# Optimization experiments

Hardware: AMD Instinct MI355X
Metric: run time of the kernel (lower is better)

## Reference

```python
import jax, jax.numpy as jnp
import numpy as np
from jax import lax

B, C_IN, C_HID, NUM_CLASSES, HW = 128, 256, 1024, 1, 17
DN = ('NCHW', 'OIHW', 'NCHW')


def setup_inputs() -> dict:
    key = jax.random.key(0)
    k = jax.random.split(key, 5)
    x = jax.random.normal(k[0], (B, C_IN, HW, HW), dtype=jnp.float32)
    # ConvRnn stand-in: 3x3 SAME conv 256->1024 + tanh (zero initial hidden state)
    w_rnn = jax.random.normal(k[1], (C_HID, C_IN, 3, 3), dtype=jnp.float32) * 0.02
    b_rnn = jax.random.normal(k[2], (C_HID,), dtype=jnp.float32) * 0.02
    # 1x1 conv 1024 -> NUM_CLASSES
    w_out = jax.random.normal(k[3], (NUM_CLASSES, C_HID, 1, 1), dtype=jnp.float32) * 0.02
    b_out = jax.random.normal(k[4], (NUM_CLASSES,), dtype=jnp.float32) * 0.02
    return {"x": x, "w_rnn": w_rnn, "b_rnn": b_rnn, "w_out": w_out, "b_out": b_out}


def _branch(x, w_rnn, b_rnn, w_out, b_out):
    h = jnp.tanh(
        lax.conv_general_dilated(x, w_rnn, (1, 1), 'SAME', dimension_numbers=DN)
        + b_rnn[None, :, None, None]
    )
    h = jax.nn.relu(h)
    s = lax.conv_general_dilated(h, w_out, (1, 1), 'SAME', dimension_numbers=DN)
    return jax.nn.sigmoid(s + b_out[None, :, None, None])  # [B, NUM_CLASSES, 17, 17]


def reference(x, w_rnn, b_rnn, w_out, b_out):
    score = _branch(x, w_rnn, b_rnn, w_out, b_out)
    # per-sample peak of channel-0 map; first occurrence in row-major order
    flat = score[:, 0].reshape(score.shape[0], -1)          # [B, H*W]
    idx = jnp.argmax(flat, axis=-1)                          # first max, like nonzero()[0]
    pos_list = jnp.stack([idx // HW, idx % HW], axis=-1).astype(jnp.int32)  # [B, 2] = (y, x)
    return (score, pos_list)
```

## Files before the change

### kernel.cpp

```cpp
#include <hip/hip_runtime.h>
#include <hip/hip_bf16.h>

#define HW_ 17
#define P_ 289
#define BIMG 128
#define CIN 256
#define CHID 1024

#define WS_ZERO_OFF 0
#define WS_S_OFF    1024
#define WS_W2_OFF   262144
#define WS_X2_OFF   9699328

typedef __attribute__((ext_vector_type(8))) short short8;
typedef __attribute__((ext_vector_type(4))) float float4_t;

__device__ __forceinline__ unsigned short f32_to_bf16_rne(float f) {
  unsigned int u = __builtin_bit_cast(unsigned int, f);
  unsigned int r = (u + 0x7FFFu + ((u >> 16) & 1u)) >> 16;
  return (unsigned short)r;
}
__device__ __forceinline__ float bf16_bits_to_f32(unsigned short h) {
  unsigned int u = ((unsigned int)h) << 16;
  return __builtin_bit_cast(float, u);
}

__device__ __forceinline__ void glds16(const void* g, void* l) {
  __builtin_amdgcn_global_load_lds(
      (const __attribute__((address_space(1))) void*)g,
      (__attribute__((address_space(3))) void*)l, 16, 0, 0);
}

__global__ void prep_w_kernel(const float* __restrict__ w_rnn,
                              unsigned short* __restrict__ w2) {
  int t = blockIdx.x * 256 + threadIdx.x;
  int c = t & 255;
  int oc = (t >> 8) & 1023;
  int kyx = t >> 18;
  float w = w_rnn[(size_t)(oc * 256 + c) * 9 + kyx];
  unsigned short hi = f32_to_bf16_rne(w);
  unsigned short lo = f32_to_bf16_rne(w - bf16_bits_to_f32(hi));
  size_t base = (size_t)(kyx * 1024 + oc) * 512;
  w2[base + c] = hi;
  w2[base + 256 + c] = lo;
}

__global__ void prep_x_kernel(const float* __restrict__ x,
                              unsigned short* __restrict__ x2) {
  __shared__ unsigned short hibuf[P_ * 34];
  __shared__ unsigned short lobuf[P_ * 34];
  int n = blockIdx.y;
  int c0 = blockIdx.x * 32;
  int t = threadIdx.x;
  for (int ci = 0; ci < 32; ++ci) {
    const float* src = x + (size_t)(n * CIN + c0 + ci) * P_;
    for (int pb = 0; pb < 2; ++pb) {
      int p = pb * 256 + t;
      if (p < P_) {
        float v = src[p];
        unsigned short h = f32_to_bf16_rne(v);
        hibuf[p * 34 + ci] = h;
        lobuf[p * 34 + ci] = f32_to_bf16_rne(v - bf16_bits_to_f32(h));
      }
    }
  }
  __syncthreads();
  int ci = t & 31;
  int psub = t >> 5;
  for (int pb = 0; pb < P_; pb += 8) {
    int p = pb + psub;
    if (p < P_) {
      size_t ob = ((size_t)n * P_ + p) * 512;
      x2[ob + c0 + ci]       = hibuf[p * 34 + ci];
      x2[ob + 256 + c0 + ci] = lobuf[p * 34 + ci];
    }
  }
}

#define BM 128
#define BN 160
#define LDS_B_OFF 16384
#define LDS_TOTAL (16384 + 20480)

__global__ __launch_bounds__(256, 2) void conv_kernel(
    const unsigned short* __restrict__ w2,
    const unsigned short* __restrict__ x2,
    const float* __restrict__ b_rnn,
    const float* __restrict__ w_out,
    const char* __restrict__ zpage,
    float* __restrict__ sbuf) {
  __shared__ char lds[LDS_TOTAL];
  int t = threadIdx.x;
  int n = blockIdx.z;
  int mb = blockIdx.x;
  int nb = blockIdx.y;
  int oc0 = mb * BM;
  int pos0 = nb * BN;

  int cc = t & 7;
  int rr = t >> 3;
  int sA = cc ^ (rr & 7);
  int sB = sA;

  int pIdx[5], pyA[5], pxA[5];
#pragma unroll
  for (int i = 0; i < 5; ++i) {
    int p = pos0 + rr + 32 * i;
    pIdx[i] = p;
    int py = p / 17;
    pyA[i] = py;
    pxA[i] = p - py * 17;
  }

  const char* w2c = (const char*)w2;
  const char* x2c = (const char*)x2;
  char* ldsA_w = lds + (size_t)(t & ~63) * 16;
  char* ldsB_w = lds + LDS_B_OFF + (size_t)(t & ~63) * 16;

  int lane = t & 63;
  int wid = t >> 6;
  int wm = wid >> 1;
  int wn = wid & 1;
  int lrow = lane & 15;
  int g = lane >> 4;
  int aoff[4], boff[5];
#pragma unroll
  for (int m = 0; m < 4; ++m) {
    int row = wm * 64 + m * 16 + lrow;
    aoff[m] = row * 128 + ((g * 16) ^ ((row & 7) << 4));
  }
#pragma unroll
  for (int nf = 0; nf < 5; ++nf) {
    int row = wn * 80 + nf * 16 + lrow;
    boff[nf] = LDS_B_OFF + row * 128 + ((g * 16) ^ ((row & 7) << 4));
  }

  float4_t acc[4][5];
#pragma unroll
  for (int m = 0; m < 4; ++m)
#pragma unroll
    for (int nf = 0; nf < 5; ++nf)
      acc[m][nf] = (float4_t){0.f, 0.f, 0.f, 0.f};

  for (int kyx = 0; kyx < 9; ++kyx) {
    int ky = kyx / 3, kx = kyx - 3 * ky;
    const char* pB[5];
#pragma unroll
    for (int i = 0; i < 5; ++i) {
      int yy = pyA[i] + ky - 1;
      int xx = pxA[i] + kx - 1;
      bool ok = (pIdx[i] < P_) && (yy >= 0) && (yy < 17) && (xx >= 0) && (xx < 17);
      pB[i] = ok ? x2c + 2 * (((size_t)(n * P_ + yy * 17 + xx)) * 512 + sB * 8)
                 : (const char*)zpage;
    }
    const char* pA = w2c + 2 * (((size_t)(kyx * 1024 + oc0 + rr)) * 512 + sA * 8);

    for (int ck = 0; ck < 12; ++ck) {
      int ckA = (ck < 4) ? ck : ck - 4;
      int ckB = (ck < 8) ? ck : ck - 8;
      const char* a = pA + ckA * 128;
      glds16(a,             ldsA_w);
      glds16(a + 32768,     ldsA_w + 4096);
      glds16(a + 65536,     ldsA_w + 8192);
      glds16(a + 98304,     ldsA_w + 12288);
      int bo = ckB * 128;
      glds16(pB[0] + bo, ldsB_w);
      glds16(pB[1] + bo, ldsB_w + 4096);
      glds16(pB[2] + bo, ldsB_w + 8192);
      glds16(pB[3] + bo, ldsB_w + 12288);
      glds16(pB[4] + bo, ldsB_w + 16384);
      __syncthreads();
#pragma unroll
      for (int ks = 0; ks < 2; ++ks) {
        int kx2 = ks << 6;
        short8 af[4], bf[5];
#pragma unroll
        for (int m = 0; m < 4; ++m)
          af[m] = *(const short8*)(lds + (aoff[m] ^ kx2));
#pragma unroll
        for (int nf = 0; nf < 5; ++nf)
          bf[nf] = *(const short8*)(lds + (boff[nf] ^ kx2));
#pragma unroll
        for (int m = 0; m < 4; ++m)
#pragma unroll
          for (int nf = 0; nf < 5; ++nf)
            acc[m][nf] = __builtin_amdgcn_mfma_f32_16x16x32_bf16(
                af[m], bf[nf], acc[m][nf], 0, 0, 0);
      }
      __syncthreads();
    }
  }

  float sacc[5] = {0.f, 0.f, 0.f, 0.f, 0.f};
#pragma unroll
  for (int m = 0; m < 4; ++m) {
#pragma unroll
    for (int r = 0; r < 4; ++r) {
      int oc = oc0 + wm * 64 + m * 16 + g * 4 + r;
      float wo = w_out[oc];
      float br = b_rnn[oc];
#pragma unroll
      for (int nf = 0; nf < 5; ++nf) {
        float v = acc[m][nf][r] + br;
        float h = tanhf(v);
        h = fmaxf(h, 0.f);
        sacc[nf] = fmaf(wo, h, sacc[nf]);
      }
    }
  }
#pragma unroll
  for (int nf = 0; nf < 5; ++nf) {
    sacc[nf] += __shfl_xor(sacc[nf], 16);
    sacc[nf] += __shfl_xor(sacc[nf], 32);
  }
  if (lane < 16) {
#pragma unroll
    for (int nf = 0; nf < 5; ++nf) {
      int pos = pos0 + wn * 80 + nf * 16 + lrow;
      if (pos < P_) atomicAdd(&sbuf[n * P_ + pos], sacc[nf]);
    }
  }
}

__global__ void finalize_kernel(const float* __restrict__ sbuf,
                                const float* __restrict__ b_out,
                                float* __restrict__ out) {
  int n = blockIdx.x;
  int lane = threadIdx.x;
  float bo = b_out[0];
  float vmax = -1e30f;
  int imax = 0x7FFFFFFF;
  for (int p = lane; p < P_; p += 64) {
    float v = sbuf[n * P_ + p] + bo;
    float sg = 1.0f / (1.0f + expf(-v));
    out[n * P_ + p] = sg;
    if (sg > vmax) { vmax = sg; imax = p; }
  }
  for (int off = 32; off >= 1; off >>= 1) {
    float ov = __shfl_xor(vmax, off);
    int oi = __shfl_xor(imax, off);
    if (ov > vmax || (ov == vmax && oi < imax)) { vmax = ov; imax = oi; }
  }
  if (lane == 0) {
    int y = imax / 17;
    int xq = imax - y * 17;
    out[BIMG * P_ + n * 2 + 0] = (float)y;
    out[BIMG * P_ + n * 2 + 1] = (float)xq;
  }
}

extern "C" void kernel_launch(void* const* d_in, const int* in_sizes, int n_in,
                              void* d_out, int out_size, void* d_ws, size_t ws_size,
                              hipStream_t stream) {
  const float* x     = (const float*)d_in[0];
  const float* w_rnn = (const float*)d_in[1];
  const float* b_rnn = (const float*)d_in[2];
  const float* w_out = (const float*)d_in[3];
  const float* b_out = (const float*)d_in[4];
  char* ws = (char*)d_ws;
  unsigned short* w2 = (unsigned short*)(ws + WS_W2_OFF);
  unsigned short* x2 = (unsigned short*)(ws + WS_X2_OFF);
  float* sbuf = (float*)(ws + WS_S_OFF);
  float* out = (float*)d_out;

  hipMemsetAsync(ws, 0, WS_S_OFF + BIMG * P_ * 4, stream);
  prep_w_kernel<<<9216, 256, 0, stream>>>(w_rnn, w2);
  prep_x_kernel<<<dim3(8, 128), 256, 0, stream>>>(x, x2);
  conv_kernel<<<dim3(8, 2, 128), 256, 0, stream>>>(w2, x2, b_rnn, w_out, ws, sbuf);
  finalize_kernel<<<128, 64, 0, stream>>>(sbuf, b_out, out);
}
```

Baseline: 670.2 us.

## Stage padded input halo in LDS once per channel chunk, double-buffer weights

The conv kernel now covers all 289 output positions per block (BN 320, 128 oc). It loads a zero-padded 19x19 input halo into LDS once per channel segment and reuses it across all 9 taps by shifting row offsets, where before each tap reloaded the im2col B tile. Weight tiles are double-buffered with explicit vmcnt waits and raw barriers so the next load overlaps with MFMA, and s_setprio is raised during compute. This cuts global traffic for the input and the number of syncs. In exchange it needs 80KB of dynamic LDS and twice the accumulators, which lowers occupancy and halves the grid to 1024 blocks.

Result: faster. 611.6 us (-8.7%).

```diff
diff --git a/kernel.cpp b/kernel.cpp
--- a/kernel.cpp
+++ b/kernel.cpp
@@ -7,13 +7,18 @@
 #define CIN 256
 #define CHID 1024
 
-#define WS_ZERO_OFF 0
 #define WS_S_OFF    1024
 #define WS_W2_OFF   262144
 #define WS_X2_OFF   9699328
 
 typedef __attribute__((ext_vector_type(8))) short short8;
 typedef __attribute__((ext_vector_type(4))) float float4_t;
+
+#define BHALO_OFF  0
+#define BHALO_ROWS 384
+#define ABUF_OFF   49152
+#define ABUF_SZ    16384
+#define LDS_TOTAL  81920
 
 __device__ __forceinline__ unsigned short f32_to_bf16_rne(float f) {
   unsigned int u = __builtin_bit_cast(unsigned int, f);
@@ -24,7 +29,6 @@
   unsigned int u = ((unsigned int)h) << 16;
   return __builtin_bit_cast(float, u);
 }
-
 __device__ __forceinline__ void glds16(const void* g, void* l) {
   __builtin_amdgcn_global_load_lds(
       (const __attribute__((address_space(1))) void*)g,
@@ -77,11 +81,6 @@
   }
 }
 
-#define BM 128
-#define BN 160
-#define LDS_B_OFF 16384
-#define LDS_TOTAL (16384 + 20480)
-
 __global__ __launch_bounds__(256, 2) void conv_kernel(
     const unsigned short* __restrict__ w2,
     const unsigned short* __restrict__ x2,
@@ -89,135 +88,149 @@
     const float* __restrict__ w_out,
     const char* __restrict__ zpage,
     float* __restrict__ sbuf) {
-  __shared__ char lds[LDS_TOTAL];
-  int t = threadIdx.x;
-  int n = blockIdx.z;
-  int mb = blockIdx.x;
-  int nb = blockIdx.y;
-  int oc0 = mb * BM;
-  int pos0 = nb * BN;
-
-  int cc = t & 7;
-  int rr = t >> 3;
-  int sA = cc ^ (rr & 7);
-  int sB = sA;
-
-  int pIdx[5], pyA[5], pxA[5];
-#pragma unroll
-  for (int i = 0; i < 5; ++i) {
-    int p = pos0 + rr + 32 * i;
-    pIdx[i] = p;
-    int py = p / 17;
-    pyA[i] = py;
-    pxA[i] = p - py * 17;
-  }
+  extern __shared__ char lds[];
+  const int t = threadIdx.x;
+  const int n = blockIdx.y;
+  const int oc0 = blockIdx.x * 128;
+
+  const int lane = t & 63;
+  const int wid = t >> 6;
+  const int wm = wid >> 1, wn = wid & 1;
+  const int lrow = lane & 15, g = lane >> 4;
+
+  const int cc = t & 7;
+  const int rr = t >> 3;
+  const int sw = cc ^ (rr & 7);
 
   const char* w2c = (const char*)w2;
   const char* x2c = (const char*)x2;
-  char* ldsA_w = lds + (size_t)(t & ~63) * 16;
-  char* ldsB_w = lds + LDS_B_OFF + (size_t)(t & ~63) * 16;
-
-  int lane = t & 63;
-  int wid = t >> 6;
-  int wm = wid >> 1;
-  int wn = wid & 1;
-  int lrow = lane & 15;
-  int g = lane >> 4;
-  int aoff[4], boff[5];
-#pragma unroll
-  for (int m = 0; m < 4; ++m) {
-    int row = wm * 64 + m * 16 + lrow;
-    aoff[m] = row * 128 + ((g * 16) ^ ((row & 7) << 4));
-  }
-#pragma unroll
-  for (int nf = 0; nf < 5; ++nf) {
-    int row = wn * 80 + nf * 16 + lrow;
-    boff[nf] = LDS_B_OFF + row * 128 + ((g * 16) ^ ((row & 7) << 4));
-  }
-
-  float4_t acc[4][5];
-#pragma unroll
-  for (int m = 0; m < 4; ++m)
-#pragma unroll
-    for (int nf = 0; nf < 5; ++nf)
-      acc[m][nf] = (float4_t){0.f, 0.f, 0.f, 0.f};
-
-  for (int kyx = 0; kyx < 9; ++kyx) {
-    int ky = kyx / 3, kx = kyx - 3 * ky;
-    const char* pB[5];
-#pragma unroll
-    for (int i = 0; i < 5; ++i) {
-      int yy = pyA[i] + ky - 1;
-      int xx = pxA[i] + kx - 1;
-      bool ok = (pIdx[i] < P_) && (yy >= 0) && (yy < 17) && (xx >= 0) && (xx < 17);
-      pB[i] = ok ? x2c + 2 * (((size_t)(n * P_ + yy * 17 + xx)) * 512 + sB * 8)
-                 : (const char*)zpage;
-    }
-    const char* pA = w2c + 2 * (((size_t)(kyx * 1024 + oc0 + rr)) * 512 + sA * 8);
-
-    for (int ck = 0; ck < 12; ++ck) {
-      int ckA = (ck < 4) ? ck : ck - 4;
-      int ckB = (ck < 8) ? ck : ck - 8;
-      const char* a = pA + ckA * 128;
-      glds16(a,             ldsA_w);
-      glds16(a + 32768,     ldsA_w + 4096);
-      glds16(a + 65536,     ldsA_w + 8192);
-      glds16(a + 98304,     ldsA_w + 12288);
-      int bo = ckB * 128;
-      glds16(pB[0] + bo, ldsB_w);
-      glds16(pB[1] + bo, ldsB_w + 4096);
-      glds16(pB[2] + bo, ldsB_w + 8192);
-      glds16(pB[3] + bo, ldsB_w + 12288);
-      glds16(pB[4] + bo, ldsB_w + 16384);
-      __syncthreads();
-#pragma unroll
-      for (int ks = 0; ks < 2; ++ks) {
-        int kx2 = ks << 6;
-        short8 af[4], bf[5];
-#pragma unroll
-        for (int m = 0; m < 4; ++m)
-          af[m] = *(const short8*)(lds + (aoff[m] ^ kx2));
-#pragma unroll
-        for (int nf = 0; nf < 5; ++nf)
-          bf[nf] = *(const short8*)(lds + (boff[nf] ^ kx2));
-#pragma unroll
-        for (int m = 0; m < 4; ++m)
-#pragma unroll
-          for (int nf = 0; nf < 5; ++nf)
-            acc[m][nf] = __builtin_amdgcn_mfma_f32_16x16x32_bf16(
-                af[m], bf[nf], acc[m][nf], 0, 0, 0);
-      }
-      __syncthreads();
-    }
-  }
-
-  float sacc[5] = {0.f, 0.f, 0.f, 0.f, 0.f};
-#pragma unroll
-  for (int m = 0; m < 4; ++m) {
+  const size_t aLaneBase = (size_t)(oc0 + rr) * 1024 + sw * 16;
+  char* aDst = lds + ABUF_OFF + (t & ~63) * 16;
+  char* bDst = lds + BHALO_OFF + (t & ~63) * 16;
+
+  int pBase[12];
+#pragma unroll
+  for (int i = 0; i < 12; ++i) {
+    int h = i * 32 + rr;
+    int hy = h / 19, hx = h - hy * 19;
+    bool interior = (h < 361) && (hy >= 1) && (hy <= 17) && (hx >= 1) && (hx <= 17);
+    int p = (hy - 1) * 17 + (hx - 1);
+    pBase[i] = interior ? (int)((size_t)(n * P_ + p) * 1024 + sw * 16) : -1;
+  }
+
+  int aoff[4][2];
+#pragma unroll
+  for (int i = 0; i < 4; ++i) {
+    int row = wm * 64 + i * 16 + lrow;
+#pragma unroll
+    for (int kk = 0; kk < 2; ++kk)
+      aoff[i][kk] = ABUF_OFF + row * 128 + ((kk * 64 + g * 16) ^ ((row & 7) << 4));
+  }
+  int hb[10];
+#pragma unroll
+  for (int j = 0; j < 10; ++j) {
+    int p = wn * 160 + j * 16 + lrow;
+    int py = p / 17;
+    hb[j] = (p < P_) ? py * 19 + (p - py * 17) : 0;
+  }
+
+  float4_t acc[4][10];
+#pragma unroll
+  for (int i = 0; i < 4; ++i)
+#pragma unroll
+    for (int j = 0; j < 10; ++j) acc[i][j] = (float4_t){0.f, 0.f, 0.f, 0.f};
+
+  {
+    const char* src = w2c + aLaneBase;
+#pragma unroll
+    for (int i = 0; i < 4; ++i) glds16(src + i * 32768, aDst + i * 4096);
+  }
+
+  for (int s = 0; s < 108; ++s) {
+    int seg, rep, tap;
+    if (s < 72) { seg = s / 18; int r = s - seg * 18; rep = r / 9; tap = r - rep * 9; }
+    else        { int q = s - 72; seg = 4 + q / 9; rep = 0; tap = q - (seg - 4) * 9; }
+
+    if (rep == 0 && tap == 0) {
+#pragma unroll
+      for (int i = 0; i < 12; ++i) {
+        const char* src = (pBase[i] >= 0) ? x2c + pBase[i] + seg * 128 : zpage;
+        glds16(src, bDst + i * 4096);
+      }
+    }
+    if (s < 107) {
+      int s1 = s + 1, seg1, rep1, tap1;
+      if (s1 < 72) { seg1 = s1 / 18; int r = s1 - seg1 * 18; rep1 = r / 9; tap1 = r - rep1 * 9; }
+      else         { int q = s1 - 72; seg1 = 4 + q / 9; rep1 = 0; tap1 = q - (seg1 - 4) * 9; }
+      int aChunk1 = (seg1 < 4) ? (rep1 ? 4 + seg1 : seg1) : (seg1 - 4);
+      const char* src = w2c + aLaneBase + (size_t)tap1 * 1048576 + aChunk1 * 128;
+      char* dst = aDst + ((s1 & 1) ? ABUF_SZ : 0);
+#pragma unroll
+      for (int i = 0; i < 4; ++i) glds16(src + i * 32768, dst + i * 4096);
+      asm volatile("s_waitcnt vmcnt(4)" ::: "memory");
+    } else {
+      asm volatile("s_waitcnt vmcnt(0)" ::: "memory");
+    }
+    __builtin_amdgcn_s_barrier();
+
+    const int d = (tap / 3) * 19 + (tap - (tap / 3) * 3);
+    const int abase = (s & 1) ? ABUF_SZ : 0;
+    __builtin_amdgcn_s_setprio(1);
+#pragma unroll
+    for (int kk = 0; kk < 2; ++kk) {
+      short8 af[4];
+#pragma unroll
+      for (int i = 0; i < 4; ++i)
+        af[i] = *(const short8*)(lds + abase + aoff[i][kk]);
+#pragma unroll
+      for (int jh = 0; jh < 2; ++jh) {
+        short8 bf[5];
+#pragma unroll
+        for (int j5 = 0; j5 < 5; ++j5) {
+          int h = hb[jh * 5 + j5] + d;
+          int boff = h * 128 + ((kk * 64 + g * 16) ^ ((h & 7) << 4));
+          bf[j5] = *(const short8*)(lds + boff);
+        }
+#pragma unroll
+        for (int i = 0; i < 4; ++i)
+#pragma unroll
+          for (int j5 = 0; j5 < 5; ++j5)
+            acc[i][jh * 5 + j5] = __builtin_amdgcn_mfma_f32_16x16x32_bf16(
+                af[i], bf[j5], acc[i][jh * 5 + j5], 0, 0, 0);
+      }
+    }
+    __builtin_amdgcn_s_setprio(0);
+    __builtin_amdgcn_s_barrier();
+    asm volatile("" ::: "memory");
+  }
+
+  float sacc[10] = {0.f, 0.f, 0.f, 0.f, 0.f, 0.f, 0.f, 0.f, 0.f, 0.f};
+#pragma unroll
+  for (int i = 0; i < 4; ++i) {
 #pragma unroll
     for (int r = 0; r < 4; ++r) {
-      int oc = oc0 + wm * 64 + m * 16 + g * 4 + r;
+      int oc = oc0 + wm * 64 + i * 16 + g * 4 + r;
       float wo = w_out[oc];
       float br = b_rnn[oc];
 #pragma unroll
-      for (int nf = 0; nf < 5; ++nf) {
-        float v = acc[m][nf][r] + br;
+      for (int j = 0; j < 10; ++j) {
+        float v = acc[i][j][r] + br;
         float h = tanhf(v);
         h = fmaxf(h, 0.f);
-        sacc[nf] = fmaf(wo, h, sacc[nf]);
-      }
-    }
-  }
-#pragma unroll
-  for (int nf = 0; nf < 5; ++nf) {
-    sacc[nf] += __shfl_xor(sacc[nf], 16);
-    sacc[nf] += __shfl_xor(sacc[nf], 32);
+        sacc[j] = fmaf(wo, h, sacc[j]);
+      }
+    }
+  }
+#pragma unroll
+  for (int j = 0; j < 10; ++j) {
+    sacc[j] += __shfl_xor(sacc[j], 16);
+    sacc[j] += __shfl_xor(sacc[j], 32);
   }
   if (lane < 16) {
 #pragma unroll
-    for (int nf = 0; nf < 5; ++nf) {
-      int pos = pos0 + wn * 80 + nf * 16 + lrow;
-      if (pos < P_) atomicAdd(&sbuf[n * P_ + pos], sacc[nf]);
+    for (int j = 0; j < 10; ++j) {
+      int pos = wn * 160 + j * 16 + lrow;
+      if (pos < P_) atomicAdd(&sbuf[n * P_ + pos], sacc[j]);
     }
   }
 }
@@ -263,9 +276,12 @@
   float* sbuf = (float*)(ws + WS_S_OFF);
   float* out = (float*)d_out;
 
+  hipFuncSetAttribute((const void*)conv_kernel,
+                      hipFuncAttributeMaxDynamicSharedMemorySize, LDS_TOTAL);
+
   hipMemsetAsync(ws, 0, WS_S_OFF + BIMG * P_ * 4, stream);
   prep_w_kernel<<<9216, 256, 0, stream>>>(w_rnn, w2);
   prep_x_kernel<<<dim3(8, 128), 256, 0, stream>>>(x, x2);
-  conv_kernel<<<dim3(8, 2, 128), 256, 0, stream>>>(w2, x2, b_rnn, w_out, ws, sbuf);
+  conv_kernel<<<dim3(8, 128), 256, LDS_TOTAL, stream>>>(w2, x2, b_rnn, w_out, ws, sbuf);
   finalize_kernel<<<128, 64, 0, stream>>>(sbuf, b_out, out);
 }
```
